# Kernel tuning notes

Measured on AMD Instinct MI355X. Metric: run time of the kernel, lower is better.

## Reference

```python
import jax, jax.numpy as jnp
import numpy as np

HEADS = 8
DIM_HEAD = 64
SCALE = DIM_HEAD ** (-0.5)


def setup_inputs() -> dict:
    key = jax.random.key(0)
    ks = jax.random.split(key, 6)
    x = jax.random.normal(ks[0], (4, 2048, 1024), dtype=jnp.float32)
    context = jax.random.normal(ks[1], (4, 512, 768), dtype=jnp.float32)
    # linear weights stored as (in, out); init scaled like nn.Linear default-ish
    Wq = jax.random.normal(ks[2], (1024, 512), dtype=jnp.float32) * (1.0 / np.sqrt(1024))
    Wk = jax.random.normal(ks[3], (768, 512), dtype=jnp.float32) * (1.0 / np.sqrt(768))
    Wv = jax.random.normal(ks[4], (768, 512), dtype=jnp.float32) * (1.0 / np.sqrt(768))
    Wo = jax.random.normal(ks[5], (512, 1024), dtype=jnp.float32) * (1.0 / np.sqrt(512))
    return {"x": x, "context": context, "Wq": Wq, "Wk": Wk, "Wv": Wv, "Wo": Wo}


def reference(x, context, Wq, Wk, Wv, Wo):
    # projections: [b, i, inner], [b, j, inner]
    q = jnp.einsum('bid,de->bie', x, Wq)
    k = jnp.einsum('bjd,de->bje', context, Wk)
    v = jnp.einsum('bjd,de->bje', context, Wv)
    b, i, _ = q.shape
    j = k.shape[1]
    # split heads: [b, h, seq, c]
    q = q.reshape(b, i, HEADS, DIM_HEAD).transpose(0, 2, 1, 3)
    k = k.reshape(b, j, HEADS, DIM_HEAD).transpose(0, 2, 1, 3)
    v = v.reshape(b, j, HEADS, DIM_HEAD).transpose(0, 2, 1, 3)
    scores = jnp.einsum('bhic,bhjc->bhij', q, k) * SCALE
    attn = jax.nn.softmax(scores, axis=-1)
    out = jnp.einsum('bhij,bhjc->bhic', attn, v)  # [b, h, i, c]
    out = out.transpose(0, 2, 1, 3).reshape(b, i, HEADS * DIM_HEAD)
    return jnp.einsum('bie,ed->bid', out, Wo)
```

## Files before the change

kernel.cpp:

```cpp
#include <hip/hip_runtime.h>
#include <stdint.h>

typedef unsigned short u16;
typedef __attribute__((ext_vector_type(8))) short short8;
typedef __attribute__((ext_vector_type(4))) float f32x4;

#define MFMA16(a, b, c) __builtin_amdgcn_mfma_f32_16x16x32_bf16((a), (b), (c), 0, 0, 0)

__device__ __forceinline__ u16 f2bf(float f) {
  unsigned int u = __float_as_uint(f);
  u += 0x7FFFu + ((u >> 16) & 1u);
  return (u16)(u >> 16);
}

__device__ __forceinline__ void gload16(const u16* g, u16* lds) {
  __builtin_amdgcn_global_load_lds(
      (const __attribute__((address_space(1))) unsigned int*)g,
      (__attribute__((address_space(3))) unsigned int*)lds, 16, 0, 0);
}

__global__ void cvt_all(const float* __restrict__ x, u16* __restrict__ xb, int n4x,
                        const float* __restrict__ cx, u16* __restrict__ cb, int n4c) {
  int i = blockIdx.x * blockDim.x + threadIdx.x;
  int stride = gridDim.x * blockDim.x;
  int total = n4x + n4c;
  for (; i < total; i += stride) {
    float4 v = (i < n4x) ? ((const float4*)x)[i] : ((const float4*)cx)[i - n4x];
    ushort4 o;
    o.x = f2bf(v.x); o.y = f2bf(v.y); o.z = f2bf(v.z); o.w = f2bf(v.w);
    if (i < n4x) ((ushort4*)xb)[i] = o; else ((ushort4*)cb)[i - n4x] = o;
  }
}

__global__ void trans_all(const float* __restrict__ Wq, const float* __restrict__ Wk,
                          const float* __restrict__ Wv, const float* __restrict__ Wo,
                          u16* __restrict__ wqT, u16* __restrict__ wkvT,
                          u16* __restrict__ woT) {
  __shared__ float tile[32][33];
  int z = blockIdx.z;
  const float* src; u16* dst; int R, C; float scale = 1.0f;
  if (z == 0)      { src = Wq; dst = wqT;  R = 1024; C = 512;  scale = 0.125f; }
  else if (z == 1) { src = Wk; dst = wkvT; R = 768;  C = 512;  }
  else if (z == 2) { src = Wv; dst = wkvT + (size_t)512 * 768; R = 768; C = 512; }
  else             { src = Wo; dst = woT;  R = 512;  C = 1024; }
  int bx = blockIdx.x * 32, by = blockIdx.y * 32;
  if (bx >= C || by >= R) return;
  int tx = threadIdx.x, ty = threadIdx.y;
#pragma unroll
  for (int i = 0; i < 4; ++i)
    tile[ty + 8 * i][tx] = src[(size_t)(by + ty + 8 * i) * C + bx + tx];
  __syncthreads();
#pragma unroll
  for (int i = 0; i < 4; ++i)
    dst[(size_t)(bx + ty + 8 * i) * R + by + tx] = f2bf(tile[tx][ty + 8 * i] * scale);
}

template <int MODE>
__device__ __forceinline__ void gemm_body(const u16* __restrict__ A,
                                          const u16* __restrict__ BT,
                                          void* __restrict__ C0p,
                                          void* __restrict__ C1p,
                                          int tm, int tn, int K, int N, u16* smem) {
  u16* As = smem;
  u16* Bs = smem + 8192;
  const int t = threadIdx.x;
  const int w = t >> 6, l = t & 63, lr = l & 15, lg = l >> 4;
  const int wr = w >> 1, wc = w & 1;

  f32x4 acc[4][2];
#pragma unroll
  for (int mi = 0; mi < 4; ++mi)
#pragma unroll
    for (int ni = 0; ni < 2; ++ni) acc[mi][ni] = (f32x4){0.f, 0.f, 0.f, 0.f};

  for (int kt = 0; kt < K; kt += 64) {
#pragma unroll
    for (int p = 0; p < 4; ++p) {
      int idx = p * 256 + t, row = idx >> 3, cg = idx & 7;
      gload16(A + (size_t)(tm + row) * K + kt + ((cg ^ (row & 7)) * 8),
              As + (p * 256 + (t & 192)) * 8);
    }
#pragma unroll
    for (int pb = 0; pb < 2; ++pb) {
      int idx = pb * 256 + t, row = idx >> 3, cg = idx & 7;
      gload16(BT + (size_t)(tn + row) * K + kt + ((cg ^ (row & 7)) * 8),
              Bs + (pb * 256 + (t & 192)) * 8);
    }
    __syncthreads();
    short8 af[4][2], bf[2][2];
#pragma unroll
    for (int mi = 0; mi < 4; ++mi)
#pragma unroll
      for (int kk = 0; kk < 2; ++kk)
        af[mi][kk] = *(const short8*)
            &As[(wr * 64 + mi * 16 + lr) * 64 + (((kk * 4 + lg) ^ (lr & 7)) * 8)];
#pragma unroll
    for (int ni = 0; ni < 2; ++ni)
#pragma unroll
      for (int kk = 0; kk < 2; ++kk)
        bf[ni][kk] = *(const short8*)
            &Bs[(wc * 32 + ni * 16 + lr) * 64 + (((kk * 4 + lg) ^ (lr & 7)) * 8)];
#pragma unroll
    for (int mi = 0; mi < 4; ++mi)
#pragma unroll
      for (int ni = 0; ni < 2; ++ni) {
        acc[mi][ni] = MFMA16(af[mi][0], bf[ni][0], acc[mi][ni]);
        acc[mi][ni] = MFMA16(af[mi][1], bf[ni][1], acc[mi][ni]);
      }
    __syncthreads();
  }

  if (MODE == 2 && tn >= 512) {
    u16* tile = smem;
#pragma unroll
    for (int mi = 0; mi < 4; ++mi)
#pragma unroll
      for (int ni = 0; ni < 2; ++ni) {
        ushort4 pk;
        pk.x = f2bf(acc[mi][ni][0]); pk.y = f2bf(acc[mi][ni][1]);
        pk.z = f2bf(acc[mi][ni][2]); pk.w = f2bf(acc[mi][ni][3]);
        *(ushort4*)&tile[(wc * 32 + ni * 16 + lr) * 136 + wr * 64 + mi * 16 + lg * 4] = pk;
      }
    __syncthreads();
    int bh = ((tm >> 9) << 3) + ((tn - 512) >> 6);
    u16* dst = (u16*)C1p + (size_t)bh * 64 * 512 + (tm & 511);
#pragma unroll
    for (int p = 0; p < 4; ++p) {
      int c = (p * 256 + t) >> 4, jj = (t & 15) * 8;
      short8 v = *(const short8*)&tile[c * 136 + jj];
      *(short8*)(dst + (size_t)c * 512 + jj) = v;
    }
    return;
  }

#pragma unroll
  for (int mi = 0; mi < 4; ++mi)
#pragma unroll
    for (int ni = 0; ni < 2; ++ni)
#pragma unroll
      for (int r = 0; r < 4; ++r) {
        int rg = tm + wr * 64 + mi * 16 + lg * 4 + r;
        int cg = tn + wc * 32 + ni * 16 + lr;
        float val = acc[mi][ni][r];
        if (MODE == 0) {
          ((float*)C0p)[(size_t)rg * N + cg] = val;
        } else if (MODE == 1) {
          ((u16*)C0p)[(((size_t)(rg >> 11) * 8 + (cg >> 6)) * 2048 + (rg & 2047)) * 64 +
                      (cg & 63)] = f2bf(val);
        } else {
          ((u16*)C0p)[(((size_t)(rg >> 9) * 8 + (cg >> 6)) * 512 + (rg & 511)) * 64 +
                      (cg & 63)] = f2bf(val);
        }
      }
}

__global__ __launch_bounds__(256) void gemm_qkv(const u16* __restrict__ xb,
                                                const u16* __restrict__ wqT,
                                                u16* __restrict__ qhb,
                                                const u16* __restrict__ cb,
                                                const u16* __restrict__ wkvT,
                                                u16* __restrict__ khb,
                                                u16* __restrict__ vtb) {
  __shared__ __align__(16) u16 smem[12288];
  int gid = (int)blockIdx.x;
  gid = (gid & 7) * 96 + (gid >> 3);
  if (gid < 512) {
    gemm_body<1>(xb, wqT, qhb, nullptr, (gid >> 3) * 128, (gid & 7) * 64, 1024, 512, smem);
  } else {
    int g2 = gid - 512;
    gemm_body<2>(cb, wkvT, khb, vtb, (g2 >> 4) * 128, (g2 & 15) * 64, 768, 1024, smem);
  }
}

__global__ __launch_bounds__(256) void gemm_o(const u16* __restrict__ aob,
                                              const u16* __restrict__ woT,
                                              float* __restrict__ out) {
  __shared__ __align__(16) u16 smem[12288];
  int gid = (int)blockIdx.x;
  gid = (gid & 7) * 128 + (gid >> 3);
  gemm_body<0>(aob, woT, out, nullptr, (gid >> 4) * 128, (gid & 15) * 64, 512, 1024, smem);
}

__global__ __launch_bounds__(256) void attn_kernel(const u16* __restrict__ qhb,
                                                   const u16* __restrict__ khb,
                                                   const u16* __restrict__ vtb,
                                                   u16* __restrict__ aob) {
  __shared__ __align__(16) u16 kvb[512 * 64];
  __shared__ __align__(16) u16 pl[4][16 * 128];
  const int t = threadIdx.x, w = t >> 6, l = t & 63, i = l & 15, g = l >> 4;
  int lid = (int)blockIdx.x;
  lid = (lid & 7) * 128 + (lid >> 3);
  const int bh = lid >> 5, qt = lid & 31;
  const int i7 = i & 7;

  const u16* qp = qhb + ((size_t)bh * 2048 + qt * 64 + w * 16) * 64;
  const u16* kp = khb + (size_t)bh * 512 * 64;
  const u16* vp = vtb + (size_t)bh * 64 * 512;

  short8 qa0 = *(const short8*)(qp + (size_t)i * 64 + g * 8);
  short8 qa1 = *(const short8*)(qp + (size_t)i * 64 + 32 + g * 8);

  const int wbase = (t & 192) * 8;

#pragma unroll
  for (int p = 0; p < 16; ++p) {
    int u = p * 256 + t;
    int r = u >> 3, cg = u & 7;
    gload16(kp + (size_t)r * 64 + ((cg ^ (r & 7)) * 8), kvb + p * 2048 + wbase);
  }
  __syncthreads();

  f32x4 sc[32];
#pragma unroll
  for (int jt = 0; jt < 32; ++jt) {
    int r = jt * 16 + i;
    short8 k0 = *(const short8*)&kvb[r * 64 + ((g ^ i7) * 8)];
    short8 k1 = *(const short8*)&kvb[r * 64 + (((4 + g) ^ i7) * 8)];
    f32x4 a = (f32x4){0.f, 0.f, 0.f, 0.f};
    a = MFMA16(k0, qa0, a);
    a = MFMA16(k1, qa1, a);
    sc[jt] = a;
  }
  __syncthreads();

#pragma unroll
  for (int p = 0; p < 16; ++p) {
    int u = p * 256 + t;
    int r = u >> 6, cg = u & 63;
    gload16(vp + (size_t)r * 512 + ((cg ^ (r & 7)) * 8), kvb + p * 2048 + wbase);
  }

  f32x4 vm = sc[0];
#pragma unroll
  for (int jt = 1; jt < 32; ++jt) {
#pragma unroll
    for (int r = 0; r < 4; ++r) vm[r] = fmaxf(vm[r], sc[jt][r]);
  }
  float mx = fmaxf(fmaxf(vm[0], vm[1]), fmaxf(vm[2], vm[3]));
  mx = fmaxf(mx, __shfl_xor(mx, 16));
  mx = fmaxf(mx, __shfl_xor(mx, 32));
  float sum = 0.f;
#pragma unroll
  for (int jt = 0; jt < 32; ++jt) {
#pragma unroll
    for (int r = 0; r < 4; ++r) {
      float e = __expf(sc[jt][r] - mx);
      sc[jt][r] = e;
      sum += e;
    }
  }
  sum += __shfl_xor(sum, 16);
  sum += __shfl_xor(sum, 32);
  float inv = 1.f / sum;

  __syncthreads();

  u16* pw = pl[w];
  f32x4 oac[4];
#pragma unroll
  for (int ct = 0; ct < 4; ++ct) oac[ct] = (f32x4){0.f, 0.f, 0.f, 0.f};

#pragma unroll
  for (int c4 = 0; c4 < 4; ++c4) {
#pragma unroll
    for (int tt = 0; tt < 8; ++tt) {
      int jt = c4 * 8 + tt;
      unsigned w0, w1;
      asm("v_cvt_pk_bf16_f32 %0, %1, %2" : "=v"(w0) : "v"(sc[jt][0]), "v"(sc[jt][1]));
      asm("v_cvt_pk_bf16_f32 %0, %1, %2" : "=v"(w1) : "v"(sc[jt][2]), "v"(sc[jt][3]));
      uint2 pk2; pk2.x = w0; pk2.y = w1;
      *(uint2*)&pw[i * 128 + ((tt * 16 + g * 4) ^ (i7 * 8))] = pk2;
    }
    asm volatile("s_waitcnt lgkmcnt(0)" ::: "memory");
    __builtin_amdgcn_sched_barrier(0);
#pragma unroll
    for (int T2 = 0; T2 < 4; ++T2) {
      short8 pa = *(const short8*)&pw[i * 128 + ((T2 * 32 + g * 8) ^ (i7 * 8))];
      int jg = c4 * 16 + T2 * 4 + g;
#pragma unroll
      for (int ct = 0; ct < 4; ++ct) {
        int vr = ct * 16 + i;
        short8 vf = *(const short8*)&kvb[vr * 512 + ((jg ^ (vr & 7)) * 8)];
        oac[ct] = MFMA16(pa, vf, oac[ct]);
      }
    }
    asm volatile("" ::: "memory");
  }

  float iv[4];
#pragma unroll
  for (int r = 0; r < 4; ++r) iv[r] = __shfl(inv, (l & 48) + g * 4 + r);
  u16* op = aob + ((size_t)(bh >> 3) * 2048 + qt * 64 + w * 16) * 512 + (bh & 7) * 64;
#pragma unroll
  for (int ct = 0; ct < 4; ++ct)
#pragma unroll
    for (int r = 0; r < 4; ++r)
      op[(size_t)(g * 4 + r) * 512 + ct * 16 + i] = f2bf(oac[ct][r] * iv[r]);
}

extern "C" void kernel_launch(void* const* d_in, const int* in_sizes, int n_in,
                              void* d_out, int out_size, void* d_ws, size_t ws_size,
                              hipStream_t stream) {
  const float* x  = (const float*)d_in[0];
  const float* cx = (const float*)d_in[1];
  const float* Wq = (const float*)d_in[2];
  const float* Wk = (const float*)d_in[3];
  const float* Wv = (const float*)d_in[4];
  const float* Wo = (const float*)d_in[5];
  float* out = (float*)d_out;

  char* p = (char*)d_ws;
  u16* xb   = (u16*)p; p += (size_t)8388608 * 2;
  u16* cb   = (u16*)p; p += (size_t)1572864 * 2;
  u16* wqT  = (u16*)p; p += (size_t)524288 * 2;
  u16* wkvT = (u16*)p; p += (size_t)786432 * 2;
  u16* woT  = (u16*)p; p += (size_t)524288 * 2;
  u16* qhb  = (u16*)p; p += (size_t)4194304 * 2;
  u16* khb  = (u16*)p; p += (size_t)1048576 * 2;
  u16* vtb  = (u16*)p; p += (size_t)1048576 * 2;
  u16* aob  = (u16*)p; p += (size_t)4194304 * 2;

  cvt_all<<<2048, 256, 0, stream>>>(x, xb, 8388608 / 4, cx, cb, 1572864 / 4);
  trans_all<<<dim3(32, 32, 4), dim3(32, 8), 0, stream>>>(Wq, Wk, Wv, Wo, wqT, wkvT, woT);

  gemm_qkv<<<768, 256, 0, stream>>>(xb, wqT, qhb, cb, wkvT, khb, vtb);
  attn_kernel<<<1024, 256, 0, stream>>>(qhb, khb, vtb, aob);
  gemm_o<<<1024, 256, 0, stream>>>(aob, woT, out);
}
```

Measured before the change: 75.70 us.

## Fuse fp32-to-bf16 activation conversion into the QKV GEMM's A-tile load path

Removes the separate cvt_all kernel and its bf16 staging buffers for x and context. The QKV GEMM now streams fp32 activations straight into LDS with a swizzled layout and converts them to bf16 with v_cvt_pk_bf16_f32 when building MFMA fragments. This saves a launch plus a full write and re-read of the converted activations. In exchange the A tile doubles in LDS footprint and global read bytes, and conversion work is repeated across the N-tiles that share each A row block.

```diff
diff --git a/kernel.cpp b/kernel.cpp
--- a/kernel.cpp
+++ b/kernel.cpp
@@ -13,23 +13,10 @@
   return (u16)(u >> 16);
 }
 
-__device__ __forceinline__ void gload16(const u16* g, u16* lds) {
+__device__ __forceinline__ void gload16(const void* g, u16* lds) {
   __builtin_amdgcn_global_load_lds(
       (const __attribute__((address_space(1))) unsigned int*)g,
       (__attribute__((address_space(3))) unsigned int*)lds, 16, 0, 0);
-}
-
-__global__ void cvt_all(const float* __restrict__ x, u16* __restrict__ xb, int n4x,
-                        const float* __restrict__ cx, u16* __restrict__ cb, int n4c) {
-  int i = blockIdx.x * blockDim.x + threadIdx.x;
-  int stride = gridDim.x * blockDim.x;
-  int total = n4x + n4c;
-  for (; i < total; i += stride) {
-    float4 v = (i < n4x) ? ((const float4*)x)[i] : ((const float4*)cx)[i - n4x];
-    ushort4 o;
-    o.x = f2bf(v.x); o.y = f2bf(v.y); o.z = f2bf(v.z); o.w = f2bf(v.w);
-    if (i < n4x) ((ushort4*)xb)[i] = o; else ((ushort4*)cb)[i - n4x] = o;
-  }
 }
 
 __global__ void trans_all(const float* __restrict__ Wq, const float* __restrict__ Wk,
@@ -55,14 +42,14 @@
     dst[(size_t)(bx + ty + 8 * i) * R + by + tx] = f2bf(tile[tx][ty + 8 * i] * scale);
 }
 
-template <int MODE>
-__device__ __forceinline__ void gemm_body(const u16* __restrict__ A,
+template <int MODE, int F32A>
+__device__ __forceinline__ void gemm_body(const void* __restrict__ Ap,
                                           const u16* __restrict__ BT,
                                           void* __restrict__ C0p,
                                           void* __restrict__ C1p,
                                           int tm, int tn, int K, int N, u16* smem) {
   u16* As = smem;
-  u16* Bs = smem + 8192;
+  u16* Bs = smem + (F32A ? 16384 : 8192);
   const int t = threadIdx.x;
   const int w = t >> 6, l = t & 63, lr = l & 15, lg = l >> 4;
   const int wr = w >> 1, wc = w & 1;
@@ -74,11 +61,22 @@
     for (int ni = 0; ni < 2; ++ni) acc[mi][ni] = (f32x4){0.f, 0.f, 0.f, 0.f};
 
   for (int kt = 0; kt < K; kt += 64) {
-#pragma unroll
-    for (int p = 0; p < 4; ++p) {
-      int idx = p * 256 + t, row = idx >> 3, cg = idx & 7;
-      gload16(A + (size_t)(tm + row) * K + kt + ((cg ^ (row & 7)) * 8),
-              As + (p * 256 + (t & 192)) * 8);
+    if (F32A) {
+      const float* A = (const float*)Ap;
+#pragma unroll
+      for (int p = 0; p < 8; ++p) {
+        int idx = p * 256 + t, row = idx >> 4, u = idx & 15;
+        gload16(A + (size_t)(tm + row) * K + kt + ((u ^ ((row & 7) << 1)) * 4),
+                As + (p * 256 + (t & 192)) * 8);
+      }
+    } else {
+      const u16* A = (const u16*)Ap;
+#pragma unroll
+      for (int p = 0; p < 4; ++p) {
+        int idx = p * 256 + t, row = idx >> 3, cg = idx & 7;
+        gload16(A + (size_t)(tm + row) * K + kt + ((cg ^ (row & 7)) * 8),
+                As + (p * 256 + (t & 192)) * 8);
+      }
     }
 #pragma unroll
     for (int pb = 0; pb < 2; ++pb) {
@@ -88,12 +86,33 @@
     }
     __syncthreads();
     short8 af[4][2], bf[2][2];
-#pragma unroll
-    for (int mi = 0; mi < 4; ++mi)
-#pragma unroll
-      for (int kk = 0; kk < 2; ++kk)
-        af[mi][kk] = *(const short8*)
-            &As[(wr * 64 + mi * 16 + lr) * 64 + (((kk * 4 + lg) ^ (lr & 7)) * 8)];
+    if (F32A) {
+      const float* Af = (const float*)As;
+#pragma unroll
+      for (int mi = 0; mi < 4; ++mi)
+#pragma unroll
+        for (int kk = 0; kk < 2; ++kk) {
+          int row = wr * 64 + mi * 16 + lr;
+          int v0 = ((kk * 4 + lg) * 2) ^ ((row & 7) << 1);
+          float4 a0 = *(const float4*)&Af[row * 64 + v0 * 4];
+          float4 a1 = *(const float4*)&Af[row * 64 + v0 * 4 + 4];
+          unsigned q0, q1, q2, q3;
+          asm("v_cvt_pk_bf16_f32 %0, %1, %2" : "=v"(q0) : "v"(a0.x), "v"(a0.y));
+          asm("v_cvt_pk_bf16_f32 %0, %1, %2" : "=v"(q1) : "v"(a0.z), "v"(a0.w));
+          asm("v_cvt_pk_bf16_f32 %0, %1, %2" : "=v"(q2) : "v"(a1.x), "v"(a1.y));
+          asm("v_cvt_pk_bf16_f32 %0, %1, %2" : "=v"(q3) : "v"(a1.z), "v"(a1.w));
+          uint4 pk; pk.x = q0; pk.y = q1; pk.z = q2; pk.w = q3;
+          union { uint4 u4; short8 s8; } cvt; cvt.u4 = pk;
+          af[mi][kk] = cvt.s8;
+        }
+    } else {
+#pragma unroll
+      for (int mi = 0; mi < 4; ++mi)
+#pragma unroll
+        for (int kk = 0; kk < 2; ++kk)
+          af[mi][kk] = *(const short8*)
+              &As[(wr * 64 + mi * 16 + lr) * 64 + (((kk * 4 + lg) ^ (lr & 7)) * 8)];
+    }
 #pragma unroll
     for (int ni = 0; ni < 2; ++ni)
 #pragma unroll
@@ -154,21 +173,21 @@
       }
 }
 
-__global__ __launch_bounds__(256) void gemm_qkv(const u16* __restrict__ xb,
+__global__ __launch_bounds__(256) void gemm_qkv(const float* __restrict__ x,
                                                 const u16* __restrict__ wqT,
                                                 u16* __restrict__ qhb,
-                                                const u16* __restrict__ cb,
+                                                const float* __restrict__ cx,
                                                 const u16* __restrict__ wkvT,
                                                 u16* __restrict__ khb,
                                                 u16* __restrict__ vtb) {
-  __shared__ __align__(16) u16 smem[12288];
+  __shared__ __align__(16) u16 smem[20480];
   int gid = (int)blockIdx.x;
   gid = (gid & 7) * 96 + (gid >> 3);
   if (gid < 512) {
-    gemm_body<1>(xb, wqT, qhb, nullptr, (gid >> 3) * 128, (gid & 7) * 64, 1024, 512, smem);
+    gemm_body<1, 1>(x, wqT, qhb, nullptr, (gid >> 3) * 128, (gid & 7) * 64, 1024, 512, smem);
   } else {
     int g2 = gid - 512;
-    gemm_body<2>(cb, wkvT, khb, vtb, (g2 >> 4) * 128, (g2 & 15) * 64, 768, 1024, smem);
+    gemm_body<2, 1>(cx, wkvT, khb, vtb, (g2 >> 4) * 128, (g2 & 15) * 64, 768, 1024, smem);
   }
 }
 
@@ -178,7 +197,7 @@
   __shared__ __align__(16) u16 smem[12288];
   int gid = (int)blockIdx.x;
   gid = (gid & 7) * 128 + (gid >> 3);
-  gemm_body<0>(aob, woT, out, nullptr, (gid >> 4) * 128, (gid & 15) * 64, 512, 1024, smem);
+  gemm_body<0, 0>(aob, woT, out, nullptr, (gid >> 4) * 128, (gid & 15) * 64, 512, 1024, smem);
 }
 
 __global__ __launch_bounds__(256) void attn_kernel(const u16* __restrict__ qhb,
@@ -310,8 +329,6 @@
   float* out = (float*)d_out;
 
   char* p = (char*)d_ws;
-  u16* xb   = (u16*)p; p += (size_t)8388608 * 2;
-  u16* cb   = (u16*)p; p += (size_t)1572864 * 2;
   u16* wqT  = (u16*)p; p += (size_t)524288 * 2;
   u16* wkvT = (u16*)p; p += (size_t)786432 * 2;
   u16* woT  = (u16*)p; p += (size_t)524288 * 2;
@@ -320,10 +337,8 @@
   u16* vtb  = (u16*)p; p += (size_t)1048576 * 2;
   u16* aob  = (u16*)p; p += (size_t)4194304 * 2;
 
-  cvt_all<<<2048, 256, 0, stream>>>(x, xb, 8388608 / 4, cx, cb, 1572864 / 4);
   trans_all<<<dim3(32, 32, 4), dim3(32, 8), 0, stream>>>(Wq, Wk, Wv, Wo, wqT, wkvT, woT);
-
-  gemm_qkv<<<768, 256, 0, stream>>>(xb, wqT, qhb, cb, wkvT, khb, vtb);
+  gemm_qkv<<<768, 256, 0, stream>>>(x, wqT, qhb, cx, wkvT, khb, vtb);
   attn_kernel<<<1024, 256, 0, stream>>>(qhb, khb, vtb, aob);
   gemm_o<<<1024, 256, 0, stream>>>(aob, woT, out);
 }
```

New measurement: 77.50 us. +2.4%, slower.

## Double attention block size with separate K/V LDS buffers and fuse prep kernels

Applied to the files above, without the earlier changes.

The attention kernel now runs 512 threads (8 waves) per block covering 128 query rows. K and V live in separate LDS buffers and both are loaded up front, so each block loads K/V once for twice as many rows and two block-wide barriers disappear. The P staging buffer per wave is halved, with the PV loop chunked in 64-column pieces. The bf16 conversion and weight transpose kernels are merged into one launch to save a launch. LDS use per block rises to about 144KB, which limits occupancy to one block per CU despite the launch-bounds hint.

```diff
diff --git a/kernel.cpp b/kernel.cpp
--- a/kernel.cpp
+++ b/kernel.cpp
@@ -13,31 +13,34 @@
   return (u16)(u >> 16);
 }
 
-__device__ __forceinline__ void gload16(const u16* g, u16* lds) {
+__device__ __forceinline__ void gload16(const void* g, u16* lds) {
   __builtin_amdgcn_global_load_lds(
       (const __attribute__((address_space(1))) unsigned int*)g,
       (__attribute__((address_space(3))) unsigned int*)lds, 16, 0, 0);
 }
 
-__global__ void cvt_all(const float* __restrict__ x, u16* __restrict__ xb, int n4x,
-                        const float* __restrict__ cx, u16* __restrict__ cb, int n4c) {
-  int i = blockIdx.x * blockDim.x + threadIdx.x;
-  int stride = gridDim.x * blockDim.x;
-  int total = n4x + n4c;
-  for (; i < total; i += stride) {
-    float4 v = (i < n4x) ? ((const float4*)x)[i] : ((const float4*)cx)[i - n4x];
-    ushort4 o;
-    o.x = f2bf(v.x); o.y = f2bf(v.y); o.z = f2bf(v.z); o.w = f2bf(v.w);
-    if (i < n4x) ((ushort4*)xb)[i] = o; else ((ushort4*)cb)[i - n4x] = o;
-  }
-}
-
-__global__ void trans_all(const float* __restrict__ Wq, const float* __restrict__ Wk,
-                          const float* __restrict__ Wv, const float* __restrict__ Wo,
-                          u16* __restrict__ wqT, u16* __restrict__ wkvT,
-                          u16* __restrict__ woT) {
+__global__ void prep_all(const float* __restrict__ x, u16* __restrict__ xb, int n4x,
+                         const float* __restrict__ cx, u16* __restrict__ cb, int n4c,
+                         const float* __restrict__ Wq, const float* __restrict__ Wk,
+                         const float* __restrict__ Wv, const float* __restrict__ Wo,
+                         u16* __restrict__ wqT, u16* __restrict__ wkvT,
+                         u16* __restrict__ woT) {
   __shared__ float tile[32][33];
   int z = blockIdx.z;
+  int tx = threadIdx.x, ty = threadIdx.y;
+  if (z == 4) {
+    int bid = blockIdx.y * 32 + blockIdx.x;
+    int tid = ty * 32 + tx;
+    int idx = bid * 256 + tid, stride = 1024 * 256;
+    int total = n4x + n4c;
+    for (int i2 = idx; i2 < total; i2 += stride) {
+      float4 v = (i2 < n4x) ? ((const float4*)x)[i2] : ((const float4*)cx)[i2 - n4x];
+      ushort4 o;
+      o.x = f2bf(v.x); o.y = f2bf(v.y); o.z = f2bf(v.z); o.w = f2bf(v.w);
+      if (i2 < n4x) ((ushort4*)xb)[i2] = o; else ((ushort4*)cb)[i2 - n4x] = o;
+    }
+    return;
+  }
   const float* src; u16* dst; int R, C; float scale = 1.0f;
   if (z == 0)      { src = Wq; dst = wqT;  R = 1024; C = 512;  scale = 0.125f; }
   else if (z == 1) { src = Wk; dst = wkvT; R = 768;  C = 512;  }
@@ -45,7 +48,6 @@
   else             { src = Wo; dst = woT;  R = 512;  C = 1024; }
   int bx = blockIdx.x * 32, by = blockIdx.y * 32;
   if (bx >= C || by >= R) return;
-  int tx = threadIdx.x, ty = threadIdx.y;
 #pragma unroll
   for (int i = 0; i < 4; ++i)
     tile[ty + 8 * i][tx] = src[(size_t)(by + ty + 8 * i) * C + bx + tx];
@@ -181,32 +183,40 @@
   gemm_body<0>(aob, woT, out, nullptr, (gid >> 4) * 128, (gid & 15) * 64, 512, 1024, smem);
 }
 
-__global__ __launch_bounds__(256) void attn_kernel(const u16* __restrict__ qhb,
-                                                   const u16* __restrict__ khb,
-                                                   const u16* __restrict__ vtb,
-                                                   u16* __restrict__ aob) {
-  __shared__ __align__(16) u16 kvb[512 * 64];
-  __shared__ __align__(16) u16 pl[4][16 * 128];
+__global__ __launch_bounds__(512, 2) void attn_kernel(const u16* __restrict__ qhb,
+                                                      const u16* __restrict__ khb,
+                                                      const u16* __restrict__ vtb,
+                                                      u16* __restrict__ aob) {
+  __shared__ __align__(16) u16 kb[512 * 64];
+  __shared__ __align__(16) u16 vb[64 * 512];
+  __shared__ __align__(16) u16 pl[8][16 * 64];
   const int t = threadIdx.x, w = t >> 6, l = t & 63, i = l & 15, g = l >> 4;
   int lid = (int)blockIdx.x;
-  lid = (lid & 7) * 128 + (lid >> 3);
-  const int bh = lid >> 5, qt = lid & 31;
+  lid = (lid & 7) * 64 + (lid >> 3);
+  const int bh = lid >> 4, qh = lid & 15;
   const int i7 = i & 7;
-
-  const u16* qp = qhb + ((size_t)bh * 2048 + qt * 64 + w * 16) * 64;
+  const int row0 = qh * 128 + w * 16;
+
+  const u16* qp = qhb + ((size_t)bh * 2048 + row0) * 64;
   const u16* kp = khb + (size_t)bh * 512 * 64;
   const u16* vp = vtb + (size_t)bh * 64 * 512;
 
   short8 qa0 = *(const short8*)(qp + (size_t)i * 64 + g * 8);
   short8 qa1 = *(const short8*)(qp + (size_t)i * 64 + 32 + g * 8);
 
-  const int wbase = (t & 192) * 8;
-
-#pragma unroll
-  for (int p = 0; p < 16; ++p) {
-    int u = p * 256 + t;
-    int r = u >> 3, cg = u & 7;
-    gload16(kp + (size_t)r * 64 + ((cg ^ (r & 7)) * 8), kvb + p * 2048 + wbase);
+  const int wbase = (t & 448) * 8;
+
+#pragma unroll
+  for (int p = 0; p < 8; ++p) {
+    int s = p * 512 + t;
+    int r = s >> 3, cg = s & 7;
+    gload16(kp + (size_t)r * 64 + ((cg ^ (r & 7)) * 8), kb + p * 4096 + wbase);
+  }
+#pragma unroll
+  for (int p = 0; p < 8; ++p) {
+    int s = p * 512 + t;
+    int r = s >> 6, cg = s & 63;
+    gload16(vp + (size_t)r * 512 + ((cg ^ (r & 7)) * 8), vb + p * 4096 + wbase);
   }
   __syncthreads();
 
@@ -214,21 +224,13 @@
 #pragma unroll
   for (int jt = 0; jt < 32; ++jt) {
     int r = jt * 16 + i;
-    short8 k0 = *(const short8*)&kvb[r * 64 + ((g ^ i7) * 8)];
-    short8 k1 = *(const short8*)&kvb[r * 64 + (((4 + g) ^ i7) * 8)];
+    short8 k0 = *(const short8*)&kb[r * 64 + ((g ^ i7) * 8)];
+    short8 k1 = *(const short8*)&kb[r * 64 + (((4 + g) ^ i7) * 8)];
     f32x4 a = (f32x4){0.f, 0.f, 0.f, 0.f};
     a = MFMA16(k0, qa0, a);
     a = MFMA16(k1, qa1, a);
     sc[jt] = a;
   }
-  __syncthreads();
-
-#pragma unroll
-  for (int p = 0; p < 16; ++p) {
-    int u = p * 256 + t;
-    int r = u >> 6, cg = u & 63;
-    gload16(vp + (size_t)r * 512 + ((cg ^ (r & 7)) * 8), kvb + p * 2048 + wbase);
-  }
 
   f32x4 vm = sc[0];
 #pragma unroll
@@ -253,34 +255,32 @@
   sum += __shfl_xor(sum, 32);
   float inv = 1.f / sum;
 
-  __syncthreads();
-
   u16* pw = pl[w];
   f32x4 oac[4];
 #pragma unroll
   for (int ct = 0; ct < 4; ++ct) oac[ct] = (f32x4){0.f, 0.f, 0.f, 0.f};
 
 #pragma unroll
-  for (int c4 = 0; c4 < 4; ++c4) {
-#pragma unroll
-    for (int tt = 0; tt < 8; ++tt) {
-      int jt = c4 * 8 + tt;
+  for (int c8 = 0; c8 < 8; ++c8) {
+#pragma unroll
+    for (int tt = 0; tt < 4; ++tt) {
+      int jt = c8 * 4 + tt;
       unsigned w0, w1;
       asm("v_cvt_pk_bf16_f32 %0, %1, %2" : "=v"(w0) : "v"(sc[jt][0]), "v"(sc[jt][1]));
       asm("v_cvt_pk_bf16_f32 %0, %1, %2" : "=v"(w1) : "v"(sc[jt][2]), "v"(sc[jt][3]));
       uint2 pk2; pk2.x = w0; pk2.y = w1;
-      *(uint2*)&pw[i * 128 + ((tt * 16 + g * 4) ^ (i7 * 8))] = pk2;
+      *(uint2*)&pw[i * 64 + ((tt * 16 + g * 4) ^ (i7 * 8))] = pk2;
     }
     asm volatile("s_waitcnt lgkmcnt(0)" ::: "memory");
     __builtin_amdgcn_sched_barrier(0);
 #pragma unroll
-    for (int T2 = 0; T2 < 4; ++T2) {
-      short8 pa = *(const short8*)&pw[i * 128 + ((T2 * 32 + g * 8) ^ (i7 * 8))];
-      int jg = c4 * 16 + T2 * 4 + g;
+    for (int T2 = 0; T2 < 2; ++T2) {
+      short8 pa = *(const short8*)&pw[i * 64 + ((T2 * 32 + g * 8) ^ (i7 * 8))];
+      int jg = c8 * 8 + T2 * 4 + g;
 #pragma unroll
       for (int ct = 0; ct < 4; ++ct) {
         int vr = ct * 16 + i;
-        short8 vf = *(const short8*)&kvb[vr * 512 + ((jg ^ (vr & 7)) * 8)];
+        short8 vf = *(const short8*)&vb[vr * 512 + ((jg ^ (vr & 7)) * 8)];
         oac[ct] = MFMA16(pa, vf, oac[ct]);
       }
     }
@@ -290,7 +290,7 @@
   float iv[4];
 #pragma unroll
   for (int r = 0; r < 4; ++r) iv[r] = __shfl(inv, (l & 48) + g * 4 + r);
-  u16* op = aob + ((size_t)(bh >> 3) * 2048 + qt * 64 + w * 16) * 512 + (bh & 7) * 64;
+  u16* op = aob + ((size_t)(bh >> 3) * 2048 + row0) * 512 + (bh & 7) * 64;
 #pragma unroll
   for (int ct = 0; ct < 4; ++ct)
 #pragma unroll
@@ -320,10 +320,9 @@
   u16* vtb  = (u16*)p; p += (size_t)1048576 * 2;
   u16* aob  = (u16*)p; p += (size_t)4194304 * 2;
 
-  cvt_all<<<2048, 256, 0, stream>>>(x, xb, 8388608 / 4, cx, cb, 1572864 / 4);
-  trans_all<<<dim3(32, 32, 4), dim3(32, 8), 0, stream>>>(Wq, Wk, Wv, Wo, wqT, wkvT, woT);
-
+  prep_all<<<dim3(32, 32, 5), dim3(32, 8), 0, stream>>>(
+      x, xb, 8388608 / 4, cx, cb, 1572864 / 4, Wq, Wk, Wv, Wo, wqT, wkvT, woT);
   gemm_qkv<<<768, 256, 0, stream>>>(xb, wqT, qhb, cb, wkvT, khb, vtb);
-  attn_kernel<<<1024, 256, 0, stream>>>(qhb, khb, vtb, aob);
+  attn_kernel<<<512, 512, 0, stream>>>(qhb, khb, vtb, aob);
   gemm_o<<<1024, 256, 0, stream>>>(aob, woT, out);
 }
```

Result: faster. 67.59 us (-10.7%).
